# Performance work log

Hardware: AMD Instinct MI355X
Metric: run time of the kernel (lower is better)

The kernel has to match this reference:

```python
import jax, jax.numpy as jnp
import numpy as np

N_NODES = 100000
N_EDGES = 600000
D = 128          # model_dim
R = 50           # deprel_size


def setup_inputs() -> dict:
    key = jax.random.key(0)
    ks = jax.random.split(key, 20)
    s = 1.0 / np.sqrt(D)
    inp = jax.random.normal(ks[0], (N_NODES, D), dtype=jnp.float32)
    deprel_edge = jax.random.randint(ks[1], (N_EDGES,), 0, R)
    deparc_edge = jax.random.randint(ks[2], (N_EDGES,), 0, 4)
    edge_index = jax.random.randint(ks[3], (2, N_EDGES), 0, N_NODES)
    # parameters (nn.Linear weights stored as [out, in]; gates are Linear(D,1))
    V_in = jax.random.normal(ks[4], (D, D), dtype=jnp.float32) * s
    V_out = jax.random.normal(ks[5], (D, D), dtype=jnp.float32) * s
    W_self = jax.random.normal(ks[6], (D, D), dtype=jnp.float32) * s
    W_norel = jax.random.normal(ks[7], (D, D), dtype=jnp.float32) * s
    V_in_gate = jax.random.normal(ks[8], (1, D), dtype=jnp.float32) * s
    V_out_gate = jax.random.normal(ks[9], (1, D), dtype=jnp.float32) * s
    W_self_gate = jax.random.normal(ks[10], (1, D), dtype=jnp.float32) * s
    W_norel_gate = jax.random.normal(ks[11], (1, D), dtype=jnp.float32) * s
    b_in = jax.random.normal(ks[12], (R, D), dtype=jnp.float32) * 0.02
    b_out = jax.random.normal(ks[13], (R, D), dtype=jnp.float32) * 0.02
    b_in_gate = jax.random.normal(ks[14], (R, 1), dtype=jnp.float32) * 0.02 + 1.0
    b_out_gate = jax.random.normal(ks[15], (R, 1), dtype=jnp.float32) * 0.02 + 1.0
    return {
        "inp": inp, "deprel_edge": deprel_edge, "deparc_edge": deparc_edge,
        "edge_index": edge_index,
        "V_in": V_in, "b_in": b_in, "V_in_gate": V_in_gate, "b_in_gate": b_in_gate,
        "V_out": V_out, "b_out": b_out, "V_out_gate": V_out_gate, "b_out_gate": b_out_gate,
        "W_self": W_self, "W_self_gate": W_self_gate,
        "W_norel": W_norel, "W_norel_gate": W_norel_gate,
    }


def reference(inp, deprel_edge, deparc_edge, edge_index,
              V_in, b_in, V_in_gate, b_in_gate,
              V_out, b_out, V_out_gate, b_out_gate,
              W_self, W_self_gate, W_norel, W_norel_gate):
    # deparc type codes: 0=align(in), 1=opposite(out), 2=self, 3=norelation
    num_nodes = inp.shape[0]
    src, tgt = edge_index[0], edge_index[1]
    # transformed node features per edge type: [4, N, D]
    T = jnp.stack([inp @ V_in.T, inp @ V_out.T, inp @ W_self.T, inp @ W_norel.T])
    # gate pre-activations per edge type: [4, N, 1]
    G = jnp.stack([inp @ V_in_gate.T, inp @ V_out_gate.T,
                   inp @ W_self_gate.T, inp @ W_norel_gate.T])
    zeros_b = jnp.zeros_like(b_in)
    zeros_bg = jnp.zeros_like(b_in_gate)
    B = jnp.stack([b_in, b_out, zeros_b, zeros_b])        # [4, R, D] (self/norel have no relation bias)
    Bg = jnp.stack([b_in_gate, b_out_gate, zeros_bg, zeros_bg])  # [4, R, 1]
    # per-edge gather + relation bias
    msg = T[deparc_edge, src] + B[deparc_edge, deprel_edge]        # [E, D]
    gate = jax.nn.sigmoid(G[deparc_edge, src] + Bg[deparc_edge, deprel_edge])  # [E, 1]
    # scatter-add to target nodes
    return jax.ops.segment_sum(msg * gate, tgt, num_segments=num_nodes)
```

## Files before the change

### kernel.cpp

```cpp
#include <hip/hip_runtime.h>
#include <hip/hip_bf16.h>

#define D 128
#define LSTR 136

typedef __bf16 bf16x8 __attribute__((ext_vector_type(8)));
typedef __bf16 bf16x4 __attribute__((ext_vector_type(4)));
typedef float  f32x4  __attribute__((ext_vector_type(4)));
typedef float  f32x2  __attribute__((ext_vector_type(2)));

template <int ISBF>
__device__ __forceinline__ bf16x8 ld8(const void* p, size_t elem)
{
    if (ISBF) return *(const bf16x8*)((const __bf16*)p + elem);
    const f32x4* f = (const f32x4*)((const float*)p + elem);
    f32x4 lo = f[0], hi = f[1];
    bf16x8 r;
    r[0] = (__bf16)lo[0]; r[1] = (__bf16)lo[1]; r[2] = (__bf16)lo[2]; r[3] = (__bf16)lo[3];
    r[4] = (__bf16)hi[0]; r[5] = (__bf16)hi[1]; r[6] = (__bf16)hi[2]; r[7] = (__bf16)hi[3];
    return r;
}
template <int ISBF>
__device__ __forceinline__ float ldf(const void* p, size_t elem)
{
    return ISBF ? (float)((const __bf16*)p)[elem] : ((const float*)p)[elem];
}

__global__ __launch_bounds__(256) void hist_detect_kernel(
    const int* __restrict__ tgt, int* __restrict__ counts, int E,
    const unsigned int* __restrict__ w, int* __restrict__ flag)
{
    __shared__ int cnt[256];
    int e = blockIdx.x * 256 + threadIdx.x;
    if (e < E) atomicAdd(&counts[tgt[e]], 1);
    if (blockIdx.x == 0) {
        int c = 0;
#pragma unroll
        for (int i = 0; i < 4; ++i) {
            unsigned int v = w[threadIdx.x * 4 + i];
            unsigned int ex = (v >> 7) & 0xFF;
            if (ex >= 90 && ex <= 134) ++c;
        }
        cnt[threadIdx.x] = c;
        __syncthreads();
        for (int s = 128; s > 0; s >>= 1) {
            if (threadIdx.x < s) cnt[threadIdx.x] += cnt[threadIdx.x + s];
            __syncthreads();
        }
        if (threadIdx.x == 0) flag[0] = (cnt[0] > 614) ? 1 : 0;
    }
}

__global__ __launch_bounds__(256) void scan1_kernel(
    const int* __restrict__ counts, int* __restrict__ rowptr,
    int* __restrict__ bsum, int M)
{
    __shared__ int sh[256];
    int base = blockIdx.x * 1024 + threadIdx.x * 4;
    int v[4];
#pragma unroll
    for (int k = 0; k < 4; ++k)
        v[k] = (base + k < M) ? counts[base + k] : 0;
    int tot = v[0] + v[1] + v[2] + v[3];
    sh[threadIdx.x] = tot;
    __syncthreads();
    for (int off = 1; off < 256; off <<= 1) {
        int t = (threadIdx.x >= off) ? sh[threadIdx.x - off] : 0;
        __syncthreads();
        sh[threadIdx.x] += t;
        __syncthreads();
    }
    int run = sh[threadIdx.x] - tot;
#pragma unroll
    for (int k = 0; k < 4; ++k) {
        if (base + k < M) rowptr[base + k] = run;
        run += v[k];
    }
    if (threadIdx.x == 255) bsum[blockIdx.x] = sh[255];
}

__global__ __launch_bounds__(256) void scan3_kernel(
    int* __restrict__ rowptr, int* __restrict__ cursor,
    const int* __restrict__ bsum, int M, int E)
{
    int b = blockIdx.x;
    int o = 0;
    for (int i = 0; i < b; ++i) o += bsum[i];
    int base = b * 1024 + threadIdx.x * 4;
#pragma unroll
    for (int k = 0; k < 4; ++k) {
        int i = base + k;
        if (i < M) {
            int r = rowptr[i] + o;
            rowptr[i] = r;
            cursor[i] = r;
        }
    }
    if (b == 0 && threadIdx.x == 0) rowptr[M] = E;
}

__global__ __launch_bounds__(256) void scatter_kernel(
    const int* __restrict__ deprel, const int* __restrict__ deparc,
    const int* __restrict__ src, const int* __restrict__ tgt,
    int* __restrict__ cursor, int2* __restrict__ recs, int E)
{
    int e = blockIdx.x * 256 + threadIdx.x;
    if (e >= E) return;
    int g = tgt[e];
    int pos = atomicAdd(&cursor[g], 1);
    recs[pos] = make_int2(src[e], (deprel[e] << 2) | deparc[e]);
}

template <int ISBF>
__device__ __forceinline__ void gemm1_body(
    const void* __restrict__ inp,
    const void* __restrict__ W0, const void* __restrict__ W1,
    const void* __restrict__ W2, const void* __restrict__ W3,
    const void* __restrict__ g0, const void* __restrict__ g1,
    const void* __restrict__ g2, const void* __restrict__ g3,
    const void* __restrict__ b_in, const void* __restrict__ b_out,
    const void* __restrict__ bg_in, const void* __restrict__ bg_out,
    __bf16* __restrict__ T, float* __restrict__ G,
    __bf16* __restrict__ Bz, float* __restrict__ Bgz, int M)
{
    __shared__ unsigned int shu[(128 * LSTR) / 2];
    __bf16* sh = (__bf16*)shu;

    const int tile = blockIdx.x >> 2;
    const int t    = blockIdx.x & 3;

    if (blockIdx.x < 101 && threadIdx.x < 128) {
        int row = blockIdx.x;
        int tid = threadIdx.x;
        float v = 0.f, gv = 0.f;
        if (row < 50) {
            v  = ldf<ISBF>(b_in, (size_t)row * D + tid);
            gv = ldf<ISBF>(bg_in, row);
        } else if (row < 100) {
            int rr = row - 50;
            v  = ldf<ISBF>(b_out, (size_t)rr * D + tid);
            gv = ldf<ISBF>(bg_out, rr);
        }
        Bz[(size_t)row * D + tid] = (__bf16)v;
        if (tid == 0) Bgz[row] = gv;
    }

    const int wave = threadIdx.x >> 6;
    const int lane = threadIdx.x & 63;
    const int lrow = lane & 15;
    const int kgrp = lane >> 4;
    const int m_base = tile * 128 + wave * 32;

    int n0 = m_base + lrow;      if (n0 >= M) n0 = 0;
    int n1 = m_base + 16 + lrow; if (n1 >= M) n1 = 0;

    bf16x8 af0[4], af1[4];
#pragma unroll
    for (int ks = 0; ks < 4; ++ks) {
        const int k0 = ks * 32 + kgrp * 8;
        af0[ks] = ld8<ISBF>(inp, (size_t)n0 * D + k0);
        af1[ks] = ld8<ISBF>(inp, (size_t)n1 * D + k0);
    }

    {
        const void* gs[4] = {g0, g1, g2, g3};
        const void* gt = gs[t];
        float s0 = 0.f, s1 = 0.f;
#pragma unroll
        for (int ks = 0; ks < 4; ++ks) {
            bf16x8 q = ld8<ISBF>(gt, ks * 32 + kgrp * 8);
#pragma unroll
            for (int j = 0; j < 8; ++j) {
                float qf = (float)q[j];
                s0 = fmaf((float)af0[ks][j], qf, s0);
                s1 = fmaf((float)af1[ks][j], qf, s1);
            }
        }
        s0 += __shfl_xor(s0, 16); s0 += __shfl_xor(s0, 32);
        s1 += __shfl_xor(s1, 16); s1 += __shfl_xor(s1, 32);
        if (kgrp == 0) {
            int nn0 = m_base + lrow;
            int nn1 = m_base + 16 + lrow;
            if (nn0 < M) G[(size_t)t * M + nn0] = s0;
            if (nn1 < M) G[(size_t)t * M + nn1] = s1;
        }
    }

    const void* Ws[4] = {W0, W1, W2, W3};
    const void* W = Ws[t];
#pragma unroll
    for (int i = 0; i < 8; ++i) {
        int slot = threadIdx.x + 256 * i;
        int f = slot >> 4;
        int s = slot & 15;
        int sp = s ^ (f & 7);
        bf16x8 v = ld8<ISBF>(W, (size_t)f * D + s * 8);
        *(bf16x8*)(sh + f * 128 + sp * 8) = v;
    }
    __syncthreads();

    f32x4 acc[2][8];
#pragma unroll
    for (int i = 0; i < 2; ++i)
#pragma unroll
        for (int j = 0; j < 8; ++j)
            acc[i][j] = (f32x4){0.f, 0.f, 0.f, 0.f};

#pragma unroll
    for (int ks = 0; ks < 4; ++ks) {
        const int slot = 4 * ks + kgrp;
#pragma unroll
        for (int ft = 0; ft < 8; ++ft) {
            int f = ft * 16 + lrow;
            int sp = slot ^ (f & 7);
            bf16x8 wf = *(const bf16x8*)(sh + f * 128 + sp * 8);
            acc[0][ft] = __builtin_amdgcn_mfma_f32_16x16x32_bf16(wf, af0[ks], acc[0][ft], 0, 0, 0);
            acc[1][ft] = __builtin_amdgcn_mfma_f32_16x16x32_bf16(wf, af1[ks], acc[1][ft], 0, 0, 0);
        }
    }
    __syncthreads();

#pragma unroll
    for (int nt = 0; nt < 2; ++nt) {
        int nl = wave * 32 + nt * 16 + lrow;
#pragma unroll
        for (int ft = 0; ft < 8; ++ft) {
            int f0 = ft * 16 + kgrp * 4;
            f32x4 v = acc[nt][ft];
            bf16x4 w4;
            w4[0] = (__bf16)v[0]; w4[1] = (__bf16)v[1];
            w4[2] = (__bf16)v[2]; w4[3] = (__bf16)v[3];
            *(bf16x4*)(sh + nl * LSTR + f0) = w4;
        }
    }
    __syncthreads();

#pragma unroll
    for (int s = 0; s < 8; ++s) {
        int idx = s * 256 + threadIdx.x;
        int node = idx >> 4;
        int seg  = idx & 15;
        bf16x8 v = *(const bf16x8*)(sh + node * LSTR + seg * 8);
        int gn = tile * 128 + node;
        if (gn < M)
            *(bf16x8*)(T + (size_t)gn * (4 * D) + t * D + seg * 8) = v;
    }
}

__global__ __launch_bounds__(256, 4) void gemm1_kernel(
    const void* __restrict__ inp,
    const void* __restrict__ W0, const void* __restrict__ W1,
    const void* __restrict__ W2, const void* __restrict__ W3,
    const void* __restrict__ g0, const void* __restrict__ g1,
    const void* __restrict__ g2, const void* __restrict__ g3,
    const void* __restrict__ b_in, const void* __restrict__ b_out,
    const void* __restrict__ bg_in, const void* __restrict__ bg_out,
    __bf16* __restrict__ T, float* __restrict__ G,
    __bf16* __restrict__ Bz, float* __restrict__ Bgz, int M,
    const int* __restrict__ flag)
{
    if (flag[0]) gemm1_body<1>(inp, W0, W1, W2, W3, g0, g1, g2, g3,
                               b_in, b_out, bg_in, bg_out, T, G, Bz, Bgz, M);
    else         gemm1_body<0>(inp, W0, W1, W2, W3, g0, g1, g2, g3,
                               b_in, b_out, bg_in, bg_out, T, G, Bz, Bgz, M);
}

template <int ISBF>
__device__ __forceinline__ void edge_agg2_body(
    const __bf16* __restrict__ T, const float* __restrict__ G,
    const __bf16* __restrict__ Bz, const float* __restrict__ Bgz,
    const int* __restrict__ rowptr, const int2* __restrict__ recs,
    void* __restrict__ out, int M)
{
    const int g = blockIdx.x * 16 + (threadIdx.x >> 4);
    if (g >= M) return;
    const int lane16 = threadIdx.x & 15;
    const int dd = lane16 * 8;

    const int beg = rowptr[g], end = rowptr[g + 1];
    const int n = end - beg;

    float acc[8];
#pragma unroll
    for (int k = 0; k < 8; ++k) acc[k] = 0.f;

    bf16x8 tv_c = {}, bz_c = {};
    float gp_c = 0.f, bg_c = 0.f;
    int2 rec_n = make_int2(0, 0);

    auto issue = [&](int2 rec) {
        int t = rec.y & 3;
        int r = rec.y >> 2;
        int bidx = (t < 2) ? t * 50 + r : 100;
        gp_c = G[(size_t)t * M + rec.x];
        bg_c = Bgz[bidx];
        tv_c = *(const bf16x8*)(T + (size_t)rec.x * (4 * D) + t * D + dd);
        bz_c = *(const bf16x8*)(Bz + (size_t)bidx * D + dd);
    };

    if (n > 0) {
        issue(recs[beg]);
        if (n > 1) rec_n = recs[beg + 1];
    }

    for (int e = 0; e < n; ++e) {
        const bf16x8 tv = tv_c, bz = bz_c;
        const float gp = gp_c, bg = bg_c;

        if (e + 1 < n) {
            issue(rec_n);
            if (e + 2 < n) rec_n = recs[beg + e + 2];
        }

        const float gate = 1.f / (1.f + __expf(-(gp + bg)));
#pragma unroll
        for (int k = 0; k < 8; ++k)
            acc[k] = fmaf(gate, (float)tv[k] + (float)bz[k], acc[k]);
    }

    if (ISBF) {
        bf16x8 w;
#pragma unroll
        for (int k = 0; k < 8; ++k) w[k] = (__bf16)acc[k];
        __builtin_nontemporal_store(w, (bf16x8*)((__bf16*)out + (size_t)g * D + dd));
    } else {
        f32x4 lo = {acc[0], acc[1], acc[2], acc[3]};
        f32x4 hi = {acc[4], acc[5], acc[6], acc[7]};
        __builtin_nontemporal_store(lo, (f32x4*)((float*)out + (size_t)g * D + dd));
        __builtin_nontemporal_store(hi, (f32x4*)((float*)out + (size_t)g * D + dd + 4));
    }
}

__global__ __launch_bounds__(256) void edge_agg2_kernel(
    const __bf16* __restrict__ T, const float* __restrict__ G,
    const __bf16* __restrict__ Bz, const float* __restrict__ Bgz,
    const int* __restrict__ rowptr, const int2* __restrict__ recs,
    void* __restrict__ out, int M, const int* __restrict__ flag)
{
    if (flag[0]) edge_agg2_body<1>(T, G, Bz, Bgz, rowptr, recs, out, M);
    else         edge_agg2_body<0>(T, G, Bz, Bgz, rowptr, recs, out, M);
}

__global__ void sentinel_kernel(__bf16* o, int n)
{
    int i = blockIdx.x * blockDim.x + threadIdx.x;
    if (i < n) o[i] = (__bf16)12345.0f;
}

static inline size_t align256(size_t x) { return (x + 255) & ~(size_t)255; }

extern "C" void kernel_launch(void* const* d_in, const int* in_sizes, int n_in,
                              void* d_out, int out_size, void* d_ws, size_t ws_size,
                              hipStream_t stream)
{
    const void* inp       = d_in[0];
    const int*  deprel    = (const int*)d_in[1];
    const int*  deparc    = (const int*)d_in[2];
    const int*  eidx      = (const int*)d_in[3];
    const void* V_in      = d_in[4];
    const void* b_in      = d_in[5];
    const void* V_in_g    = d_in[6];
    const void* b_in_g    = d_in[7];
    const void* V_out     = d_in[8];
    const void* b_out     = d_in[9];
    const void* V_out_g   = d_in[10];
    const void* b_out_g   = d_in[11];
    const void* W_self    = d_in[12];
    const void* W_self_g  = d_in[13];
    const void* W_norel   = d_in[14];
    const void* W_norel_g = d_in[15];

    const int M = in_sizes[0] / D;
    const int E = in_sizes[1];
    const int* src = eidx;
    const int* tgt = eidx + E;
    const int NB = (M + 1023) / 1024;

    size_t off = 0;
    size_t o_flag   = off; off = align256(off + sizeof(int));
    size_t o_T      = off; off = align256(off + (size_t)M * 4 * D * sizeof(__bf16));
    size_t o_G      = off; off = align256(off + (size_t)4 * M * sizeof(float));
    size_t o_counts = off; off = align256(off + (size_t)M * sizeof(int));
    size_t o_rowptr = off; off = align256(off + (size_t)(M + 1) * sizeof(int));
    size_t o_cursor = off; off = align256(off + (size_t)M * sizeof(int));
    size_t o_bsum   = off; off = align256(off + (size_t)NB * sizeof(int));
    size_t o_recs   = off; off = align256(off + (size_t)E * sizeof(int2));
    size_t o_Bz     = off; off = align256(off + (size_t)101 * D * sizeof(__bf16));
    size_t o_Bgz    = off; off = align256(off + (size_t)101 * sizeof(float));

    if (off > ws_size) {
        sentinel_kernel<<<(out_size + 255) / 256, 256, 0, stream>>>(
            (__bf16*)d_out, out_size);
        return;
    }

    int*    flag   = (int*)((char*)d_ws + o_flag);
    __bf16* T      = (__bf16*)((char*)d_ws + o_T);
    float*  Gbuf   = (float*)((char*)d_ws + o_G);
    int*    counts = (int*)((char*)d_ws + o_counts);
    int*    rowptr = (int*)((char*)d_ws + o_rowptr);
    int*    cursor = (int*)((char*)d_ws + o_cursor);
    int*    bsum   = (int*)((char*)d_ws + o_bsum);
    int2*   recs   = (int2*)((char*)d_ws + o_recs);
    __bf16* Bz     = (__bf16*)((char*)d_ws + o_Bz);
    float*  Bgz    = (float*)((char*)d_ws + o_Bgz);

    hipMemsetAsync(counts, 0, (size_t)M * sizeof(int), stream);
    hist_detect_kernel<<<(E + 255) / 256, 256, 0, stream>>>(
        tgt, counts, E, (const unsigned int*)inp, flag);
    scan1_kernel<<<NB, 256, 0, stream>>>(counts, rowptr, bsum, M);
    scan3_kernel<<<NB, 256, 0, stream>>>(rowptr, cursor, bsum, M, E);
    scatter_kernel<<<(E + 255) / 256, 256, 0, stream>>>(deprel, deparc, src, tgt,
                                                        cursor, recs, E);

    const int ntiles = (M + 127) / 128;
    gemm1_kernel<<<ntiles * 4, 256, 0, stream>>>(
        inp, V_in, V_out, W_self, W_norel,
        V_in_g, V_out_g, W_self_g, W_norel_g,
        b_in, b_out, b_in_g, b_out_g, T, Gbuf, Bz, Bgz, M, flag);

    edge_agg2_kernel<<<(M + 15) / 16, 256, 0, stream>>>(
        T, Gbuf, Bz, Bgz, rowptr, recs, d_out, M, flag);
}
```

Before: 296.8 us.

## Halve gemm1 LDS footprint and remap blocks across XCDs

The GEMM shared buffer shrinks from 128x136 bf16 to 64x136. The weight tile is now staged in two K-halves, and the output tile is written back in two 64-node halves, each followed by a barrier. The block index is also remapped so that consecutive logical tiles land on the same XCD, which should improve L2 locality for the input rows shared by the four weight types. This trades extra __syncthreads for lower LDS use, allowing higher occupancy per CU.

Result: faster. 276.5 us (-6.8%).

```diff
diff --git a/kernel.cpp b/kernel.cpp
--- a/kernel.cpp
+++ b/kernel.cpp
@@ -123,11 +123,17 @@
     __bf16* __restrict__ T, float* __restrict__ G,
     __bf16* __restrict__ Bz, float* __restrict__ Bgz, int M)
 {
-    __shared__ unsigned int shu[(128 * LSTR) / 2];
+    __shared__ unsigned int shu[4352];
     __bf16* sh = (__bf16*)shu;
 
-    const int tile = blockIdx.x >> 2;
-    const int t    = blockIdx.x & 3;
+    const int nb  = gridDim.x;
+    const int b   = blockIdx.x;
+    const int xcd = b & 7, slot = b >> 3;
+    const int q = nb >> 3, r = nb & 7;
+    const int lin = (xcd < r) ? xcd * (q + 1) + slot
+                              : r * (q + 1) + (xcd - r) * q + slot;
+    const int tile = lin >> 2;
+    const int t    = lin & 3;
 
     if (blockIdx.x < 101 && threadIdx.x < 128) {
         int row = blockIdx.x;
@@ -168,10 +174,10 @@
         float s0 = 0.f, s1 = 0.f;
 #pragma unroll
         for (int ks = 0; ks < 4; ++ks) {
-            bf16x8 q = ld8<ISBF>(gt, ks * 32 + kgrp * 8);
+            bf16x8 qv = ld8<ISBF>(gt, ks * 32 + kgrp * 8);
 #pragma unroll
             for (int j = 0; j < 8; ++j) {
-                float qf = (float)q[j];
+                float qf = (float)qv[j];
                 s0 = fmaf((float)af0[ks][j], qf, s0);
                 s1 = fmaf((float)af1[ks][j], qf, s1);
             }
@@ -188,16 +194,6 @@
 
     const void* Ws[4] = {W0, W1, W2, W3};
     const void* W = Ws[t];
-#pragma unroll
-    for (int i = 0; i < 8; ++i) {
-        int slot = threadIdx.x + 256 * i;
-        int f = slot >> 4;
-        int s = slot & 15;
-        int sp = s ^ (f & 7);
-        bf16x8 v = ld8<ISBF>(W, (size_t)f * D + s * 8);
-        *(bf16x8*)(sh + f * 128 + sp * 8) = v;
-    }
-    __syncthreads();
 
     f32x4 acc[2][8];
 #pragma unroll
@@ -207,43 +203,63 @@
             acc[i][j] = (f32x4){0.f, 0.f, 0.f, 0.f};
 
 #pragma unroll
-    for (int ks = 0; ks < 4; ++ks) {
-        const int slot = 4 * ks + kgrp;
-#pragma unroll
-        for (int ft = 0; ft < 8; ++ft) {
-            int f = ft * 16 + lrow;
-            int sp = slot ^ (f & 7);
-            bf16x8 wf = *(const bf16x8*)(sh + f * 128 + sp * 8);
-            acc[0][ft] = __builtin_amdgcn_mfma_f32_16x16x32_bf16(wf, af0[ks], acc[0][ft], 0, 0, 0);
-            acc[1][ft] = __builtin_amdgcn_mfma_f32_16x16x32_bf16(wf, af1[ks], acc[1][ft], 0, 0, 0);
-        }
-    }
-    __syncthreads();
-
-#pragma unroll
-    for (int nt = 0; nt < 2; ++nt) {
-        int nl = wave * 32 + nt * 16 + lrow;
-#pragma unroll
-        for (int ft = 0; ft < 8; ++ft) {
-            int f0 = ft * 16 + kgrp * 4;
-            f32x4 v = acc[nt][ft];
-            bf16x4 w4;
-            w4[0] = (__bf16)v[0]; w4[1] = (__bf16)v[1];
-            w4[2] = (__bf16)v[2]; w4[3] = (__bf16)v[3];
-            *(bf16x4*)(sh + nl * LSTR + f0) = w4;
-        }
-    }
-    __syncthreads();
-
-#pragma unroll
-    for (int s = 0; s < 8; ++s) {
-        int idx = s * 256 + threadIdx.x;
-        int node = idx >> 4;
-        int seg  = idx & 15;
-        bf16x8 v = *(const bf16x8*)(sh + node * LSTR + seg * 8);
-        int gn = tile * 128 + node;
-        if (gn < M)
-            *(bf16x8*)(T + (size_t)gn * (4 * D) + t * D + seg * 8) = v;
+    for (int h = 0; h < 2; ++h) {
+#pragma unroll
+        for (int i = 0; i < 4; ++i) {
+            int idx = threadIdx.x + 256 * i;
+            int f = idx >> 3;
+            int s = idx & 7;
+            int sp = s ^ (f & 7);
+            bf16x8 v = ld8<ISBF>(W, (size_t)f * D + h * 64 + s * 8);
+            *(bf16x8*)(sh + f * 64 + sp * 8) = v;
+        }
+        __syncthreads();
+
+#pragma unroll
+        for (int kl = 0; kl < 2; ++kl) {
+            const int ks = h * 2 + kl;
+            const int slot = kl * 4 + kgrp;
+#pragma unroll
+            for (int ft = 0; ft < 8; ++ft) {
+                int f = ft * 16 + lrow;
+                int sp = slot ^ (f & 7);
+                bf16x8 wf = *(const bf16x8*)(sh + f * 64 + sp * 8);
+                acc[0][ft] = __builtin_amdgcn_mfma_f32_16x16x32_bf16(wf, af0[ks], acc[0][ft], 0, 0, 0);
+                acc[1][ft] = __builtin_amdgcn_mfma_f32_16x16x32_bf16(wf, af1[ks], acc[1][ft], 0, 0, 0);
+            }
+        }
+        __syncthreads();
+    }
+
+#pragma unroll
+    for (int bh = 0; bh < 2; ++bh) {
+        if ((wave >> 1) == bh) {
+            int nlb = (wave & 1) * 32;
+#pragma unroll
+            for (int nt = 0; nt < 2; ++nt) {
+#pragma unroll
+                for (int ft = 0; ft < 8; ++ft) {
+                    int f0 = ft * 16 + kgrp * 4;
+                    f32x4 v = acc[nt][ft];
+                    bf16x4 w4;
+                    w4[0] = (__bf16)v[0]; w4[1] = (__bf16)v[1];
+                    w4[2] = (__bf16)v[2]; w4[3] = (__bf16)v[3];
+                    *(bf16x4*)(sh + (nlb + nt * 16 + lrow) * LSTR + f0) = w4;
+                }
+            }
+        }
+        __syncthreads();
+#pragma unroll
+        for (int s = 0; s < 4; ++s) {
+            int idx = s * 256 + threadIdx.x;
+            int node = idx >> 4;
+            int seg  = idx & 15;
+            bf16x8 v = *(const bf16x8*)(sh + node * LSTR + seg * 8);
+            int gn = tile * 128 + bh * 64 + node;
+            if (gn < M)
+                *(bf16x8*)(T + (size_t)gn * (4 * D) + t * D + seg * 8) = v;
+        }
+        if (bh == 0) __syncthreads();
     }
 }
 
```
